# Kernel optimization log

Hardware: AMD Instinct MI355X
Metric: run time of the kernel (lower is better)

The kernel has to match this reference:

```python
import jax, jax.numpy as jnp
import numpy as np

D_MODEL = 1024
NUM_HEADS = 16
HEAD_DIM = D_MODEL // NUM_HEADS  # 64
ROPE_BASE = 10000.0


def setup_inputs() -> dict:
    key = jax.random.key(0)
    ks = jax.random.split(key, 12)
    B, S, D = 4, 2048, D_MODEL
    scale = 1.0 / np.sqrt(D)
    inp = {
        'query': jax.random.normal(ks[0], (B, S, D), jnp.float32),
        'key': jax.random.normal(ks[1], (B, S, D), jnp.float32),
        'value': jax.random.normal(ks[2], (B, S, D), jnp.float32),
        'Wq': jax.random.normal(ks[3], (D, D), jnp.float32) * scale,
        'bq': jnp.zeros((D,), jnp.float32),
        'Wk': jax.random.normal(ks[4], (D, D), jnp.float32) * scale,
        'bk': jnp.zeros((D,), jnp.float32),
        'Wv': jax.random.normal(ks[5], (D, D), jnp.float32) * scale,
        'bv': jnp.zeros((D,), jnp.float32),
        'Wo': jax.random.normal(ks[6], (D, D), jnp.float32) * scale,
        'bo': jnp.zeros((D,), jnp.float32),
    }
    return inp


def _rope_cos_sin(seq_len, head_dim, dtype):
    inv_freq = 1.0 / (ROPE_BASE ** (jnp.arange(0, head_dim, 2, dtype=jnp.float32) / head_dim))
    t = jnp.arange(seq_len, dtype=jnp.float32)
    freqs = jnp.einsum('i,j->ij', t, inv_freq)          # [S, hd/2]
    emb = jnp.concatenate([freqs, freqs], axis=-1)      # [S, hd]
    return jnp.cos(emb).astype(dtype), jnp.sin(emb).astype(dtype)


def _rotate_half(x):
    x1, x2 = jnp.split(x, 2, axis=-1)
    return jnp.concatenate([-x2, x1], axis=-1)


def reference(query, key, value, Wq, bq, Wk, bk, Wv, bv, Wo, bo):
    B, T, D = query.shape
    H, hd = NUM_HEADS, HEAD_DIM
    # projections -> [B, H, S, hd]
    Q = (query @ Wq + bq).reshape(B, T, H, hd).transpose(0, 2, 1, 3)
    K = (key @ Wk + bk).reshape(B, -1, H, hd).transpose(0, 2, 1, 3)
    V = (value @ Wv + bv).reshape(B, -1, H, hd).transpose(0, 2, 1, 3)
    # RoPE
    cos, sin = _rope_cos_sin(T, hd, Q.dtype)            # [S, hd]
    Q = Q * cos + _rotate_half(Q) * sin
    K = K * cos + _rotate_half(K) * sin
    # attention
    scores = jnp.einsum('bhtd,bhsd->bhts', Q, K) / jnp.sqrt(jnp.asarray(hd, Q.dtype))
    attn = jax.nn.softmax(scores, axis=-1)
    context = jnp.einsum('bhts,bhsd->bhtd', attn, V)
    context = context.transpose(0, 2, 1, 3).reshape(B, T, D)
    return context @ Wo + bo
```

## Files before the change

### kernel.cpp

```cpp
#include <hip/hip_runtime.h>
#include <hip/hip_bf16.h>
#include <cstdint>
#include <cstddef>

typedef __bf16 bf16_t;
typedef __bf16 bf16x8 __attribute__((ext_vector_type(8)));
typedef __bf16 bf16x4v __attribute__((ext_vector_type(4)));
typedef float f32x4 __attribute__((ext_vector_type(4)));

#define DEVI static __device__ __forceinline__

DEVI void gl_lds16(const void* g, void* l) {
    __builtin_amdgcn_global_load_lds((const __attribute__((address_space(1))) void*)g,
                                     (__attribute__((address_space(3))) void*)l, 16, 0, 0);
}

DEVI float rsum16(float v) {
    v += __shfl_xor(v, 1);
    v += __shfl_xor(v, 2);
    v += __shfl_xor(v, 4);
    v += __shfl_xor(v, 8);
    return v;
}

DEVI float fexp2(float x) {
#if __has_builtin(__builtin_amdgcn_exp2f)
    return __builtin_amdgcn_exp2f(x);
#else
    return __expf(x * 0.6931471805599453f);
#endif
}

__global__ __launch_bounds__(256) void castk(const float* __restrict__ in, bf16_t* __restrict__ out) {
    size_t i = ((size_t)blockIdx.x * 256 + threadIdx.x) * 4;
    float4 v = *(const float4*)(in + i);
    bf16x4v o;
    o[0] = (bf16_t)v.x; o[1] = (bf16_t)v.y; o[2] = (bf16_t)v.z; o[3] = (bf16_t)v.w;
    *(bf16x4v*)(out + i) = o;
}

__global__ __launch_bounds__(256) void wtrans(const float* __restrict__ W0, const float* __restrict__ W1,
                                              const float* __restrict__ W2, const float* __restrict__ W3,
                                              bf16_t* __restrict__ O0, bf16_t* __restrict__ O1,
                                              bf16_t* __restrict__ O2, bf16_t* __restrict__ O3) {
    const float* W; bf16_t* O;
    switch (blockIdx.z) {
        case 0: W = W0; O = O0; break;
        case 1: W = W1; O = O1; break;
        case 2: W = W2; O = O2; break;
        default: W = W3; O = O3; break;
    }
    __shared__ float t[32][33];
    int tx = threadIdx.x & 31, ty = threadIdx.x >> 5;
    int bx = blockIdx.x * 32, by = blockIdx.y * 32;
#pragma unroll
    for (int yy = 0; yy < 4; ++yy)
        t[ty + yy * 8][tx] = W[(size_t)(by + ty + yy * 8) * 1024 + bx + tx];
    __syncthreads();
#pragma unroll
    for (int yy = 0; yy < 4; ++yy)
        O[(size_t)(bx + ty + yy * 8) * 1024 + by + tx] = (bf16_t)t[tx][ty + yy * 8];
}

__global__ __launch_bounds__(256) void rope_tab(float* __restrict__ ctab, float* __restrict__ stab) {
    int idx = blockIdx.x * 256 + threadIdx.x;
    int s = idx >> 5, i = idx & 31;
    float inv = 1.0f / powf(10000.0f, (float)i * (1.0f / 32.0f));
    float f = (float)s * inv;
    ctab[idx] = cosf(f);
    stab[idx] = sinf(f);
}

template <int MODE>
__global__ __launch_bounds__(256) void gemm_bt(const bf16_t* __restrict__ A, const bf16_t* __restrict__ Bt,
                                               const float* __restrict__ bias, void* __restrict__ Cout,
                                               const float* __restrict__ ctab, const float* __restrict__ stab,
                                               float scale) {
    constexpr int K = 1024, N = 1024;
    __shared__ alignas(16) bf16_t As[128 * 32];
    __shared__ alignas(16) bf16_t Bs[128 * 32];
    const int tid = threadIdx.x;
    const int w = tid >> 6, lane = tid & 63, c = lane & 15, qd = lane >> 4;
    const int wm = w >> 1, wn = w & 1;
    const int m0 = blockIdx.y * 128, n0 = blockIdx.x * 128;
    f32x4 acc[4][4] = {};
    for (int kt = 0; kt < K / 32; ++kt) {
#pragma unroll
        for (int l = 0; l < 2; ++l) {
            int e = (l * 256 + tid) * 8;
            int row = e >> 5, col = e & 31;
            gl_lds16(A + (size_t)(m0 + row) * K + kt * 32 + col, (char*)As + (size_t)e * 2);
            gl_lds16(Bt + (size_t)(n0 + row) * K + kt * 32 + col, (char*)Bs + (size_t)e * 2);
        }
        __syncthreads();
        bf16x8 af[4], bfr[4];
#pragma unroll
        for (int i = 0; i < 4; ++i) af[i] = *(const bf16x8*)&As[(wm * 64 + i * 16 + c) * 32 + qd * 8];
#pragma unroll
        for (int j = 0; j < 4; ++j) bfr[j] = *(const bf16x8*)&Bs[(wn * 64 + j * 16 + c) * 32 + qd * 8];
#pragma unroll
        for (int i = 0; i < 4; ++i)
#pragma unroll
            for (int j = 0; j < 4; ++j)
                acc[i][j] = __builtin_amdgcn_mfma_f32_16x16x32_bf16(af[i], bfr[j], acc[i][j], 0, 0, 0);
        __syncthreads();
    }
    const int mb = m0 + wm * 64;
    const int nb = n0 + wn * 64;
    if constexpr (MODE == 2) {
        float* O = (float*)Cout;
#pragma unroll
        for (int i = 0; i < 4; ++i)
#pragma unroll
            for (int j = 0; j < 4; ++j) {
                int n = nb + j * 16 + c;
                float bv = bias[n];
#pragma unroll
                for (int r = 0; r < 4; ++r) {
                    int m = mb + i * 16 + qd * 4 + r;
                    O[(size_t)m * N + n] = acc[i][j][r] + bv;
                }
            }
    } else if constexpr (MODE == 3) {
        bf16_t* O = (bf16_t*)Cout;
        int h = nb >> 6;
#pragma unroll
        for (int i = 0; i < 4; ++i) {
            int m = mb + i * 16 + qd * 4;
            int b = m >> 11, s = m & 2047;
#pragma unroll
            for (int j = 0; j < 4; ++j) {
                int d = j * 16 + c;
                float bv = bias[nb + d];
                bf16x4v v4;
#pragma unroll
                for (int r = 0; r < 4; ++r) v4[r] = (bf16_t)(acc[i][j][r] + bv);
                *(bf16x4v*)((bf16_t*)O + ((size_t)(b * 16 + h) * 64 + d) * 2048 + s) = v4;
            }
        }
    } else {
        bf16_t* O = (bf16_t*)Cout;
        int h = nb >> 6;
#pragma unroll
        for (int i = 0; i < 4; ++i)
#pragma unroll
            for (int jh = 0; jh < 2; ++jh) {
                int d1 = jh * 16 + c;
                float b1 = bias[nb + d1];
                float b2 = bias[nb + d1 + 32];
#pragma unroll
                for (int r = 0; r < 4; ++r) {
                    int m = mb + i * 16 + qd * 4 + r;
                    int b = m >> 11, s = m & 2047;
                    float v1 = acc[i][jh][r] + b1;
                    float v2 = acc[i][jh + 2][r] + b2;
                    float ct = ctab[s * 32 + d1];
                    float st = stab[s * 32 + d1];
                    size_t base = ((size_t)(b * 16 + h) * 2048 + s) * 64;
                    O[base + d1]      = (bf16_t)((v1 * ct - v2 * st) * scale);
                    O[base + d1 + 32] = (bf16_t)((v2 * ct + v1 * st) * scale);
                }
            }
    }
}

__global__ __launch_bounds__(256) void attn(const bf16_t* __restrict__ Q, const bf16_t* __restrict__ K,
                                            const bf16_t* __restrict__ Vt, bf16_t* __restrict__ ctx) {
    constexpr int S = 2048;
    __shared__ alignas(16) bf16_t Qs[128 * 64];
    __shared__ alignas(16) bf16_t Ks[64 * 64];
    __shared__ alignas(16) bf16_t Vts[64 * 64];
    __shared__ alignas(16) bf16_t Ps[4][32 * 64];
    const int tid = threadIdx.x, w = tid >> 6, lane = tid & 63, c = lane & 15, qd = lane >> 4;
    const int bh = blockIdx.y, q0 = blockIdx.x * 128;
    const bf16_t* Qb = Q + (size_t)bh * S * 64 + (size_t)q0 * 64;
    const bf16_t* Kb = K + (size_t)bh * S * 64;
    const bf16_t* Vb = Vt + (size_t)bh * 64 * S;
#pragma unroll
    for (int l = 0; l < 4; ++l) {
        int slot = l * 256 + tid;
        int row = slot >> 3, ch = slot & 7;
        int sch = ch ^ ((row >> 1) & 7);
        gl_lds16(Qb + (size_t)row * 64 + sch * 8, (char*)Qs + (size_t)slot * 16);
    }
    f32x4 acc_o[2][4] = {};
    float l_st[2][4] = {};
    const int rch = (c >> 1) & 7;
    __syncthreads();
    for (int kt = 0; kt < S / 64; ++kt) {
        const int s0 = kt * 64;
#pragma unroll
        for (int l = 0; l < 2; ++l) {
            int slot = l * 256 + tid;
            int row = slot >> 3, ch = slot & 7;
            int sch = ch ^ ((row >> 1) & 7);
            gl_lds16(Kb + (size_t)(s0 + row) * 64 + sch * 8, (char*)Ks + (size_t)slot * 16);
            gl_lds16(Vb + (size_t)row * S + s0 + sch * 8, (char*)Vts + (size_t)slot * 16);
        }
        __syncthreads();
        f32x4 sc[2][4] = {};
#pragma unroll
        for (int kk = 0; kk < 2; ++kk) {
            const int ch = (4 * kk + qd) ^ rch;
            bf16x8 af[2], bfr[4];
#pragma unroll
            for (int i = 0; i < 2; ++i) af[i] = *(const bf16x8*)&Qs[(w * 32 + i * 16 + c) * 64 + ch * 8];
#pragma unroll
            for (int j = 0; j < 4; ++j) bfr[j] = *(const bf16x8*)&Ks[(j * 16 + c) * 64 + ch * 8];
#pragma unroll
            for (int i = 0; i < 2; ++i)
#pragma unroll
                for (int j = 0; j < 4; ++j)
                    sc[i][j] = __builtin_amdgcn_mfma_f32_16x16x32_bf16(af[i], bfr[j], sc[i][j], 0, 0, 0);
        }
#pragma unroll
        for (int i = 0; i < 2; ++i)
#pragma unroll
            for (int r = 0; r < 4; ++r) {
                int rowp = i * 16 + qd * 4 + r;
                int msk = (rowp >> 1) & 7;
                float rs = 0.f;
#pragma unroll
                for (int j = 0; j < 4; ++j) {
                    float p = fexp2(sc[i][j][r]);
                    rs += p;
                    int ch = (2 * j + (c >> 3)) ^ msk;
                    Ps[w][rowp * 64 + ch * 8 + (c & 7)] = (bf16_t)p;
                }
                l_st[i][r] += rs;
            }
#pragma unroll
        for (int kk = 0; kk < 2; ++kk) {
            const int ch = (4 * kk + qd) ^ rch;
            bf16x8 pf[2], vf[4];
#pragma unroll
            for (int i = 0; i < 2; ++i) pf[i] = *(const bf16x8*)&Ps[w][(i * 16 + c) * 64 + ch * 8];
#pragma unroll
            for (int j = 0; j < 4; ++j) vf[j] = *(const bf16x8*)&Vts[(j * 16 + c) * 64 + ch * 8];
#pragma unroll
            for (int i = 0; i < 2; ++i)
#pragma unroll
                for (int j = 0; j < 4; ++j)
                    acc_o[i][j] = __builtin_amdgcn_mfma_f32_16x16x32_bf16(pf[i], vf[j], acc_o[i][j], 0, 0, 0);
        }
        __syncthreads();
    }
    float linv[2][4];
#pragma unroll
    for (int i = 0; i < 2; ++i)
#pragma unroll
        for (int r = 0; r < 4; ++r) linv[i][r] = 1.0f / rsum16(l_st[i][r]);
    const int b = bh >> 4, h = bh & 15;
#pragma unroll
    for (int i = 0; i < 2; ++i)
#pragma unroll
        for (int j = 0; j < 4; ++j)
#pragma unroll
            for (int r = 0; r < 4; ++r) {
                int qrow = q0 + w * 32 + i * 16 + qd * 4 + r;
                float o = acc_o[i][j][r] * linv[i][r];
                ctx[((size_t)(b * 2048 + qrow)) * 1024 + (size_t)h * 64 + j * 16 + c] = (bf16_t)o;
            }
}

extern "C" void kernel_launch(void* const* d_in, const int* in_sizes, int n_in,
                              void* d_out, int out_size, void* d_ws, size_t ws_size,
                              hipStream_t stream) {
    (void)in_sizes; (void)n_in; (void)out_size; (void)ws_size;
    const float* query = (const float*)d_in[0];
    const float* key   = (const float*)d_in[1];
    const float* value = (const float*)d_in[2];
    const float* Wq = (const float*)d_in[3];
    const float* bq = (const float*)d_in[4];
    const float* Wk = (const float*)d_in[5];
    const float* bk = (const float*)d_in[6];
    const float* Wv = (const float*)d_in[7];
    const float* bv = (const float*)d_in[8];
    const float* Wo = (const float*)d_in[9];
    const float* bo = (const float*)d_in[10];

    const size_t SZ = (size_t)8192 * 1024;
    bf16_t* Xq = (bf16_t*)d_ws;
    bf16_t* Xk = Xq + SZ;
    bf16_t* Xv = Xk + SZ;
    bf16_t* Qb = Xv + SZ;
    bf16_t* Kb = Qb + SZ;
    bf16_t* spare = Kb + SZ;
    bf16_t* Wqt = spare + SZ;
    bf16_t* Wkt = Wqt + 1024 * 1024;
    bf16_t* Wvt = Wkt + 1024 * 1024;
    bf16_t* Wot = Wvt + 1024 * 1024;
    float* ctab = (float*)(Wot + 1024 * 1024);
    float* stab = ctab + 2048 * 32;
    bf16_t* Vtb = Xk;
    bf16_t* CT  = Xq;

    castk<<<8192, 256, 0, stream>>>(query, Xq);
    castk<<<8192, 256, 0, stream>>>(key, Xk);
    castk<<<8192, 256, 0, stream>>>(value, Xv);
    wtrans<<<dim3(32, 32, 4), 256, 0, stream>>>(Wq, Wk, Wv, Wo, Wqt, Wkt, Wvt, Wot);
    rope_tab<<<256, 256, 0, stream>>>(ctab, stab);
    gemm_bt<0><<<dim3(8, 64), 256, 0, stream>>>(Xq, Wqt, bq, Qb, ctab, stab, 0.18033688011112042f);
    gemm_bt<0><<<dim3(8, 64), 256, 0, stream>>>(Xk, Wkt, bk, Kb, ctab, stab, 1.0f);
    gemm_bt<3><<<dim3(8, 64), 256, 0, stream>>>(Xv, Wvt, bv, Vtb, nullptr, nullptr, 1.0f);
    attn<<<dim3(16, 64), 256, 0, stream>>>(Qb, Kb, Vtb, CT);
    gemm_bt<2><<<dim3(8, 64), 256, 0, stream>>>(CT, Wot, bo, d_out, nullptr, nullptr, 1.0f);
}
```

Baseline: 404.3 us.

## Batch QKV GEMMs and casts, double-buffer K/V and keep P in registers

Merges the three cast kernels and the three projection GEMMs into single launches with a z/y grid dimension, so launches are fewer and each grid fills more CUs. The attention kernel now double-buffers K/V tiles in LDS, prefetching the next tile while the current one is computed, and keeps Q fragments in registers. It computes S^T so the bf16 P fragments can be moved with cross-lane shuffles instead of a round trip through LDS. This removes the P shared buffer and a barrier phase, in exchange for many shuffles, higher register pressure and a new launch bound of 3 blocks per CU.

```diff
diff --git a/kernel.cpp b/kernel.cpp
--- a/kernel.cpp
+++ b/kernel.cpp
@@ -6,21 +6,15 @@
 typedef __bf16 bf16_t;
 typedef __bf16 bf16x8 __attribute__((ext_vector_type(8)));
 typedef __bf16 bf16x4v __attribute__((ext_vector_type(4)));
+typedef __bf16 bf16x2v __attribute__((ext_vector_type(2)));
 typedef float f32x4 __attribute__((ext_vector_type(4)));
+typedef uint32_t u32x4 __attribute__((ext_vector_type(4)));
 
 #define DEVI static __device__ __forceinline__
 
 DEVI void gl_lds16(const void* g, void* l) {
     __builtin_amdgcn_global_load_lds((const __attribute__((address_space(1))) void*)g,
                                      (__attribute__((address_space(3))) void*)l, 16, 0, 0);
-}
-
-DEVI float rsum16(float v) {
-    v += __shfl_xor(v, 1);
-    v += __shfl_xor(v, 2);
-    v += __shfl_xor(v, 4);
-    v += __shfl_xor(v, 8);
-    return v;
 }
 
 DEVI float fexp2(float x) {
@@ -31,7 +25,18 @@
 #endif
 }
 
-__global__ __launch_bounds__(256) void castk(const float* __restrict__ in, bf16_t* __restrict__ out) {
+DEVI uint32_t pkbf16(float a, float b) {
+    bf16x2v t;
+    t[0] = (bf16_t)a;
+    t[1] = (bf16_t)b;
+    return __builtin_bit_cast(uint32_t, t);
+}
+
+__global__ __launch_bounds__(256) void castk(const float* __restrict__ i0, const float* __restrict__ i1,
+                                             const float* __restrict__ i2, bf16_t* __restrict__ o0,
+                                             bf16_t* __restrict__ o1, bf16_t* __restrict__ o2) {
+    const float* in = blockIdx.y == 0 ? i0 : blockIdx.y == 1 ? i1 : i2;
+    bf16_t* out = blockIdx.y == 0 ? o0 : blockIdx.y == 1 ? o1 : o2;
     size_t i = ((size_t)blockIdx.x * 256 + threadIdx.x) * 4;
     float4 v = *(const float4*)(in + i);
     bf16x4v o;
@@ -71,12 +76,21 @@
     stab[idx] = sinf(f);
 }
 
-template <int MODE>
-__global__ __launch_bounds__(256) void gemm_bt(const bf16_t* __restrict__ A, const bf16_t* __restrict__ Bt,
-                                               const float* __restrict__ bias, void* __restrict__ Cout,
-                                               const float* __restrict__ ctab, const float* __restrict__ stab,
-                                               float scale) {
-    constexpr int K = 1024, N = 1024;
+__global__ __launch_bounds__(256) void gemm_qkv(const bf16_t* __restrict__ Xq, const bf16_t* __restrict__ Xk,
+                                                const bf16_t* __restrict__ Xv, const bf16_t* __restrict__ Wqt,
+                                                const bf16_t* __restrict__ Wkt, const bf16_t* __restrict__ Wvt,
+                                                const float* __restrict__ bqp, const float* __restrict__ bkp,
+                                                const float* __restrict__ bvp, bf16_t* __restrict__ Qo,
+                                                bf16_t* __restrict__ Ko, bf16_t* __restrict__ Vo,
+                                                const float* __restrict__ ctab, const float* __restrict__ stab) {
+    constexpr int K = 1024;
+    const int z = blockIdx.z;
+    const bf16_t* A  = z == 0 ? Xq : z == 1 ? Xk : Xv;
+    const bf16_t* Bt = z == 0 ? Wqt : z == 1 ? Wkt : Wvt;
+    const float* bias = z == 0 ? bqp : z == 1 ? bkp : bvp;
+    bf16_t* O = z == 0 ? Qo : z == 1 ? Ko : Vo;
+    const float scale = z == 0 ? 0.18033688011112042f : 1.0f;
+
     __shared__ alignas(16) bf16_t As[128 * 32];
     __shared__ alignas(16) bf16_t Bs[128 * 32];
     const int tid = threadIdx.x;
@@ -107,23 +121,8 @@
     }
     const int mb = m0 + wm * 64;
     const int nb = n0 + wn * 64;
-    if constexpr (MODE == 2) {
-        float* O = (float*)Cout;
-#pragma unroll
-        for (int i = 0; i < 4; ++i)
-#pragma unroll
-            for (int j = 0; j < 4; ++j) {
-                int n = nb + j * 16 + c;
-                float bv = bias[n];
-#pragma unroll
-                for (int r = 0; r < 4; ++r) {
-                    int m = mb + i * 16 + qd * 4 + r;
-                    O[(size_t)m * N + n] = acc[i][j][r] + bv;
-                }
-            }
-    } else if constexpr (MODE == 3) {
-        bf16_t* O = (bf16_t*)Cout;
-        int h = nb >> 6;
+    const int h = nb >> 6;
+    if (z == 2) {
 #pragma unroll
         for (int i = 0; i < 4; ++i) {
             int m = mb + i * 16 + qd * 4;
@@ -135,12 +134,10 @@
                 bf16x4v v4;
 #pragma unroll
                 for (int r = 0; r < 4; ++r) v4[r] = (bf16_t)(acc[i][j][r] + bv);
-                *(bf16x4v*)((bf16_t*)O + ((size_t)(b * 16 + h) * 64 + d) * 2048 + s) = v4;
+                *(bf16x4v*)(O + ((size_t)(b * 16 + h) * 64 + d) * 2048 + s) = v4;
             }
         }
     } else {
-        bf16_t* O = (bf16_t*)Cout;
-        int h = nb >> 6;
 #pragma unroll
         for (int i = 0; i < 4; ++i)
 #pragma unroll
@@ -164,13 +161,58 @@
     }
 }
 
-__global__ __launch_bounds__(256) void attn(const bf16_t* __restrict__ Q, const bf16_t* __restrict__ K,
-                                            const bf16_t* __restrict__ Vt, bf16_t* __restrict__ ctx) {
+__global__ __launch_bounds__(256) void gemm_out(const bf16_t* __restrict__ A, const bf16_t* __restrict__ Bt,
+                                                const float* __restrict__ bias, float* __restrict__ O) {
+    constexpr int K = 1024, N = 1024;
+    __shared__ alignas(16) bf16_t As[128 * 32];
+    __shared__ alignas(16) bf16_t Bs[128 * 32];
+    const int tid = threadIdx.x;
+    const int w = tid >> 6, lane = tid & 63, c = lane & 15, qd = lane >> 4;
+    const int wm = w >> 1, wn = w & 1;
+    const int m0 = blockIdx.y * 128, n0 = blockIdx.x * 128;
+    f32x4 acc[4][4] = {};
+    for (int kt = 0; kt < K / 32; ++kt) {
+#pragma unroll
+        for (int l = 0; l < 2; ++l) {
+            int e = (l * 256 + tid) * 8;
+            int row = e >> 5, col = e & 31;
+            gl_lds16(A + (size_t)(m0 + row) * K + kt * 32 + col, (char*)As + (size_t)e * 2);
+            gl_lds16(Bt + (size_t)(n0 + row) * K + kt * 32 + col, (char*)Bs + (size_t)e * 2);
+        }
+        __syncthreads();
+        bf16x8 af[4], bfr[4];
+#pragma unroll
+        for (int i = 0; i < 4; ++i) af[i] = *(const bf16x8*)&As[(wm * 64 + i * 16 + c) * 32 + qd * 8];
+#pragma unroll
+        for (int j = 0; j < 4; ++j) bfr[j] = *(const bf16x8*)&Bs[(wn * 64 + j * 16 + c) * 32 + qd * 8];
+#pragma unroll
+        for (int i = 0; i < 4; ++i)
+#pragma unroll
+            for (int j = 0; j < 4; ++j)
+                acc[i][j] = __builtin_amdgcn_mfma_f32_16x16x32_bf16(af[i], bfr[j], acc[i][j], 0, 0, 0);
+        __syncthreads();
+    }
+    const int mb = m0 + wm * 64, nb = n0 + wn * 64;
+#pragma unroll
+    for (int i = 0; i < 4; ++i)
+#pragma unroll
+        for (int j = 0; j < 4; ++j) {
+            int n = nb + j * 16 + c;
+            float bv = bias[n];
+#pragma unroll
+            for (int r = 0; r < 4; ++r) {
+                int m = mb + i * 16 + qd * 4 + r;
+                O[(size_t)m * N + n] = acc[i][j][r] + bv;
+            }
+        }
+}
+
+__global__ __launch_bounds__(256, 3) void attn(const bf16_t* __restrict__ Q, const bf16_t* __restrict__ K,
+                                               const bf16_t* __restrict__ Vt, bf16_t* __restrict__ ctx) {
     constexpr int S = 2048;
     __shared__ alignas(16) bf16_t Qs[128 * 64];
-    __shared__ alignas(16) bf16_t Ks[64 * 64];
-    __shared__ alignas(16) bf16_t Vts[64 * 64];
-    __shared__ alignas(16) bf16_t Ps[4][32 * 64];
+    __shared__ alignas(16) bf16_t Ks[2][64 * 64];
+    __shared__ alignas(16) bf16_t Vts[2][64 * 64];
     const int tid = threadIdx.x, w = tid >> 6, lane = tid & 63, c = lane & 15, qd = lane >> 4;
     const int bh = blockIdx.y, q0 = blockIdx.x * 128;
     const bf16_t* Qb = Q + (size_t)bh * S * 64 + (size_t)q0 * 64;
@@ -183,73 +225,105 @@
         int sch = ch ^ ((row >> 1) & 7);
         gl_lds16(Qb + (size_t)row * 64 + sch * 8, (char*)Qs + (size_t)slot * 16);
     }
-    f32x4 acc_o[2][4] = {};
-    float l_st[2][4] = {};
-    const int rch = (c >> 1) & 7;
-    __syncthreads();
-    for (int kt = 0; kt < S / 64; ++kt) {
+    auto stageKV = [&](int kt, int buf) {
         const int s0 = kt * 64;
 #pragma unroll
         for (int l = 0; l < 2; ++l) {
             int slot = l * 256 + tid;
             int row = slot >> 3, ch = slot & 7;
             int sch = ch ^ ((row >> 1) & 7);
-            gl_lds16(Kb + (size_t)(s0 + row) * 64 + sch * 8, (char*)Ks + (size_t)slot * 16);
-            gl_lds16(Vb + (size_t)row * S + s0 + sch * 8, (char*)Vts + (size_t)slot * 16);
-        }
-        __syncthreads();
-        f32x4 sc[2][4] = {};
+            gl_lds16(Kb + (size_t)(s0 + row) * 64 + sch * 8, (char*)&Ks[buf][0] + (size_t)slot * 16);
+            gl_lds16(Vb + (size_t)row * S + s0 + sch * 8, (char*)&Vts[buf][0] + (size_t)slot * 16);
+        }
+    };
+    stageKV(0, 0);
+    const int rch = (c >> 1) & 7;
+    const int srcA = c + ((lane >> 4) & 1) * 32;
+    const int srcB = srcA + 16;
+    const bool hisel = (qd >> 1) & 1;
+    f32x4 acc_o[2][4] = {};
+    float ls[2] = {0.f, 0.f};
+    const f32x4 Z = {0.f, 0.f, 0.f, 0.f};
+    __syncthreads();
+    bf16x8 qf[2][2];
+#pragma unroll
+    for (int kk = 0; kk < 2; ++kk) {
+        const int ch = (4 * kk + qd) ^ rch;
+#pragma unroll
+        for (int i = 0; i < 2; ++i)
+            qf[kk][i] = *(const bf16x8*)&Qs[(w * 32 + i * 16 + c) * 64 + ch * 8];
+    }
+    for (int kt = 0; kt < S / 64; ++kt) {
+        const int cur = kt & 1;
+        if (kt + 1 < S / 64) stageKV(kt + 1, cur ^ 1);
+        f32x4 sc[4][2];
 #pragma unroll
         for (int kk = 0; kk < 2; ++kk) {
             const int ch = (4 * kk + qd) ^ rch;
-            bf16x8 af[2], bfr[4];
-#pragma unroll
-            for (int i = 0; i < 2; ++i) af[i] = *(const bf16x8*)&Qs[(w * 32 + i * 16 + c) * 64 + ch * 8];
-#pragma unroll
-            for (int j = 0; j < 4; ++j) bfr[j] = *(const bf16x8*)&Ks[(j * 16 + c) * 64 + ch * 8];
-#pragma unroll
-            for (int i = 0; i < 2; ++i)
-#pragma unroll
-                for (int j = 0; j < 4; ++j)
-                    sc[i][j] = __builtin_amdgcn_mfma_f32_16x16x32_bf16(af[i], bfr[j], sc[i][j], 0, 0, 0);
-        }
-#pragma unroll
-        for (int i = 0; i < 2; ++i)
-#pragma unroll
-            for (int r = 0; r < 4; ++r) {
-                int rowp = i * 16 + qd * 4 + r;
-                int msk = (rowp >> 1) & 7;
-                float rs = 0.f;
-#pragma unroll
-                for (int j = 0; j < 4; ++j) {
-                    float p = fexp2(sc[i][j][r]);
-                    rs += p;
-                    int ch = (2 * j + (c >> 3)) ^ msk;
-                    Ps[w][rowp * 64 + ch * 8 + (c & 7)] = (bf16_t)p;
-                }
-                l_st[i][r] += rs;
+            bf16x8 kf[4];
+#pragma unroll
+            for (int j = 0; j < 4; ++j) kf[j] = *(const bf16x8*)&Ks[cur][(j * 16 + c) * 64 + ch * 8];
+#pragma unroll
+            for (int j = 0; j < 4; ++j)
+#pragma unroll
+                for (int i = 0; i < 2; ++i)
+                    sc[j][i] = __builtin_amdgcn_mfma_f32_16x16x32_bf16(kf[j], qf[kk][i],
+                                                                       kk == 0 ? Z : sc[j][i], 0, 0, 0);
+        }
+        uint32_t pku[4][2][2];
+#pragma unroll
+        for (int j = 0; j < 4; ++j)
+#pragma unroll
+            for (int i = 0; i < 2; ++i) {
+                float p0 = fexp2(sc[j][i][0]), p1 = fexp2(sc[j][i][1]);
+                float p2 = fexp2(sc[j][i][2]), p3 = fexp2(sc[j][i][3]);
+                ls[i] += (p0 + p1) + (p2 + p3);
+                pku[j][i][0] = pkbf16(p0, p1);
+                pku[j][i][1] = pkbf16(p2, p3);
             }
 #pragma unroll
         for (int kk = 0; kk < 2; ++kk) {
             const int ch = (4 * kk + qd) ^ rch;
-            bf16x8 pf[2], vf[4];
-#pragma unroll
-            for (int i = 0; i < 2; ++i) pf[i] = *(const bf16x8*)&Ps[w][(i * 16 + c) * 64 + ch * 8];
-#pragma unroll
-            for (int j = 0; j < 4; ++j) vf[j] = *(const bf16x8*)&Vts[(j * 16 + c) * 64 + ch * 8];
-#pragma unroll
-            for (int i = 0; i < 2; ++i)
+            bf16x8 vf[4];
+#pragma unroll
+            for (int j = 0; j < 4; ++j) vf[j] = *(const bf16x8*)&Vts[cur][(j * 16 + c) * 64 + ch * 8];
+#pragma unroll
+            for (int i = 0; i < 2; ++i) {
+                uint32_t a0, a1, a2, a3;
+                {
+                    uint32_t lo = __shfl(pku[2 * kk][i][0], srcA);
+                    uint32_t hi = __shfl(pku[2 * kk + 1][i][0], srcA);
+                    a0 = hisel ? hi : lo;
+                    lo = __shfl(pku[2 * kk][i][1], srcA);
+                    hi = __shfl(pku[2 * kk + 1][i][1], srcA);
+                    a1 = hisel ? hi : lo;
+                    lo = __shfl(pku[2 * kk][i][0], srcB);
+                    hi = __shfl(pku[2 * kk + 1][i][0], srcB);
+                    a2 = hisel ? hi : lo;
+                    lo = __shfl(pku[2 * kk][i][1], srcB);
+                    hi = __shfl(pku[2 * kk + 1][i][1], srcB);
+                    a3 = hisel ? hi : lo;
+                }
+                u32x4 av = {a0, a1, a2, a3};
+                bf16x8 af = __builtin_bit_cast(bf16x8, av);
 #pragma unroll
                 for (int j = 0; j < 4; ++j)
-                    acc_o[i][j] = __builtin_amdgcn_mfma_f32_16x16x32_bf16(pf[i], vf[j], acc_o[i][j], 0, 0, 0);
+                    acc_o[i][j] = __builtin_amdgcn_mfma_f32_16x16x32_bf16(af, vf[j], acc_o[i][j], 0, 0, 0);
+            }
         }
         __syncthreads();
     }
     float linv[2][4];
 #pragma unroll
-    for (int i = 0; i < 2; ++i)
-#pragma unroll
-        for (int r = 0; r < 4; ++r) linv[i][r] = 1.0f / rsum16(l_st[i][r]);
+    for (int i = 0; i < 2; ++i) {
+        float v = ls[i];
+        v += __shfl_xor(v, 16);
+        v += __shfl_xor(v, 32);
+        float vinv = 1.0f / v;
+#pragma unroll
+        for (int r = 0; r < 4; ++r)
+            linv[i][r] = __shfl(vinv, qd * 20 + r);
+    }
     const int b = bh >> 4, h = bh & 15;
 #pragma unroll
     for (int i = 0; i < 2; ++i)
@@ -285,24 +359,20 @@
     bf16_t* Xv = Xk + SZ;
     bf16_t* Qb = Xv + SZ;
     bf16_t* Kb = Qb + SZ;
-    bf16_t* spare = Kb + SZ;
-    bf16_t* Wqt = spare + SZ;
+    bf16_t* Vtb = Kb + SZ;
+    bf16_t* Wqt = Vtb + SZ;
     bf16_t* Wkt = Wqt + 1024 * 1024;
     bf16_t* Wvt = Wkt + 1024 * 1024;
     bf16_t* Wot = Wvt + 1024 * 1024;
     float* ctab = (float*)(Wot + 1024 * 1024);
     float* stab = ctab + 2048 * 32;
-    bf16_t* Vtb = Xk;
-    bf16_t* CT  = Xq;
-
-    castk<<<8192, 256, 0, stream>>>(query, Xq);
-    castk<<<8192, 256, 0, stream>>>(key, Xk);
-    castk<<<8192, 256, 0, stream>>>(value, Xv);
+    bf16_t* CT = Xq;
+
+    castk<<<dim3(8192, 3), 256, 0, stream>>>(query, key, value, Xq, Xk, Xv);
     wtrans<<<dim3(32, 32, 4), 256, 0, stream>>>(Wq, Wk, Wv, Wo, Wqt, Wkt, Wvt, Wot);
     rope_tab<<<256, 256, 0, stream>>>(ctab, stab);
-    gemm_bt<0><<<dim3(8, 64), 256, 0, stream>>>(Xq, Wqt, bq, Qb, ctab, stab, 0.18033688011112042f);
-    gemm_bt<0><<<dim3(8, 64), 256, 0, stream>>>(Xk, Wkt, bk, Kb, ctab, stab, 1.0f);
-    gemm_bt<3><<<dim3(8, 64), 256, 0, stream>>>(Xv, Wvt, bv, Vtb, nullptr, nullptr, 1.0f);
+    gemm_qkv<<<dim3(8, 64, 3), 256, 0, stream>>>(Xq, Xk, Xv, Wqt, Wkt, Wvt, bq, bk, bv,
+                                                 Qb, Kb, Vtb, ctab, stab);
     attn<<<dim3(16, 64), 256, 0, stream>>>(Qb, Kb, Vtb, CT);
-    gemm_bt<2><<<dim3(8, 64), 256, 0, stream>>>(CT, Wot, bo, d_out, nullptr, nullptr, 1.0f);
-}
+    gemm_out<<<dim3(8, 64), 256, 0, stream>>>(CT, Wot, bo, (float*)d_out);
+}
```

Result: faster. 387.2 us (-4.2%).
